# Optimization experiments

Hardware: AMD Instinct MI355X
Metric: run time of the kernel (lower is better)

Reference implementation:

```python
import jax, jax.numpy as jnp
import numpy as np

N, C_IN, T, V, M = 2048, 16, 8, 21, 2
C_OUT = 64
VM = V * M                       # 42 = n_joints
NUM_NODES = N * T * VM           # 688128 flattened nodes
NUM_HEDGES = NUM_NODES           # hyperedge ids drawn from same range
E_INC = 4 * NUM_NODES            # incidence (node, hyperedge) pairs
EMBED = VM * C_OUT // 8          # 336
HEADS = 4
HEAD_DIM = EMBED // HEADS        # 84


def setup_inputs() -> dict:
    key = jax.random.key(0)
    ks = jax.random.split(key, 16)
    g = lambda k, s: jax.random.normal(k, s, jnp.float32) * 0.02
    return dict(
        x=jax.random.normal(ks[0], (N, C_IN, T, V, M), jnp.float32),
        hi=jax.random.randint(ks[1], (2, E_INC), 0, NUM_NODES, jnp.int32),
        hc_w=g(ks[2], (C_OUT, C_IN)), hc_b=jnp.zeros((C_OUT,), jnp.float32),
        conv_w=g(ks[3], (8, 8)), conv_b=jnp.zeros((8,), jnp.float32),
        bn_gamma=jnp.ones((C_IN,), jnp.float32), bn_beta=jnp.zeros((C_IN,), jnp.float32),
        proj_w=g(ks[4], (C_OUT, C_IN)), proj_b=jnp.zeros((C_OUT,), jnp.float32),
        wq=g(ks[5], (EMBED, EMBED)), bq=jnp.zeros((EMBED,), jnp.float32),
        wk=g(ks[6], (EMBED, EMBED)), bk=jnp.zeros((EMBED,), jnp.float32),
        wv=g(ks[7], (EMBED, EMBED)), bv=jnp.zeros((EMBED,), jnp.float32),
        in_proj_w=g(ks[8], (3 * EMBED, EMBED)), in_proj_b=jnp.zeros((3 * EMBED,), jnp.float32),
        out_proj_w=g(ks[9], (EMBED, EMBED)), out_proj_b=jnp.zeros((EMBED,), jnp.float32),
        fc_w=g(ks[10], (8 * EMBED, EMBED)), fc_b=jnp.zeros((8 * EMBED,), jnp.float32),
    )


def _forward(x, hi, hc_w, hc_b, conv_w, conv_b, bn_gamma, bn_beta, proj_w, proj_b,
             wq, bq, wk, bk, wv, bv, in_proj_w, in_proj_b, out_proj_w, out_proj_b,
             fc_w, fc_b):
    # ---- residual branch: rearrange n c t v m -> n c (vm) t, BN (train-mode batch stats), proj ----
    res = x.reshape(N, C_IN, T, VM).transpose(0, 1, 3, 2)          # [N,C,VM,T]
    mean = res.mean(axis=(0, 2, 3), keepdims=True)
    var = ((res - mean) ** 2).mean(axis=(0, 2, 3), keepdims=True)
    res = (res - mean) * jax.lax.rsqrt(var + 1e-5)
    res = res * bn_gamma[None, :, None, None] + bn_beta[None, :, None, None]
    res = res.transpose(0, 3, 2, 1)                                 # n t vm c
    res = res @ proj_w.T + proj_b                                   # [N,T,VM,C_OUT]
    res = res.reshape(N, T, VM * C_OUT)                             # [N,8,2688]

    # ---- HypergraphConv (PyG math: D^-1 H B H^T X Theta + bias) ----
    xn = x.transpose(0, 2, 3, 4, 1).reshape(NUM_NODES, C_IN)        # (n t v m) c
    xt = xn @ hc_w.T                                                # [Nn, C_OUT]
    node_idx, edge_idx = hi[0], hi[1]
    ones = jnp.ones((E_INC,), xt.dtype)
    D = jax.ops.segment_sum(ones, node_idx, NUM_NODES)
    Dinv = jnp.where(D > 0, 1.0 / D, 0.0)
    Bd = jax.ops.segment_sum(ones, edge_idx, NUM_HEDGES)
    Binv = jnp.where(Bd > 0, 1.0 / Bd, 0.0)
    e = jax.ops.segment_sum(Binv[edge_idx, None] * xt[node_idx], edge_idx, NUM_HEDGES)
    h = jax.ops.segment_sum(Dinv[node_idx, None] * e[edge_idx], node_idx, NUM_NODES)
    h = h + hc_b                                                    # [Nn, C_OUT]

    # torch .view(N,-1,T,V,M) is a raw reshape of the (nodes, C) buffer
    h = h.reshape(N, C_OUT, T, V, M)
    h = h.transpose(0, 2, 3, 4, 1).reshape(N, T, VM, C_OUT)         # n t vm c

    # ---- Conv2d(8->8, k=(1,1), stride=(1,8)) over channel dim T ----
    hs = h[:, :, :, ::8]                                            # [N,8,VM,8]
    hc2 = jnp.einsum('oi,nivw->novw', conv_w, hs) + conv_b[None, :, None, None]
    seq = hc2.transpose(0, 1, 3, 2).reshape(N, 8, EMBED)            # n t (c vm) -> [N,8,336]

    # ---- external QKV projections + nn.MultiheadAttention ----
    q = seq @ wq.T + bq
    k = seq @ wk.T + bk
    v = seq @ wv.T + bv
    qq = q @ in_proj_w[:EMBED].T + in_proj_b[:EMBED]
    kk = k @ in_proj_w[EMBED:2 * EMBED].T + in_proj_b[EMBED:2 * EMBED]
    vv = v @ in_proj_w[2 * EMBED:].T + in_proj_b[2 * EMBED:]
    qq = qq.reshape(N, 8, HEADS, HEAD_DIM)
    kk = kk.reshape(N, 8, HEADS, HEAD_DIM)
    vv = vv.reshape(N, 8, HEADS, HEAD_DIM)
    scores = jnp.einsum('nshd,nthd->nhst', qq, kk) / np.sqrt(HEAD_DIM).astype(np.float32)
    attn = jax.nn.softmax(scores, axis=-1)
    ao = jnp.einsum('nhst,nthd->nshd', attn, vv).reshape(N, 8, EMBED)
    ao = ao @ out_proj_w.T + out_proj_b

    out = ao @ fc_w.T + fc_b                                        # [N,8,8*EMBED=2688]
    out = jax.nn.relu(out + res)
    return out.reshape(N, 64, T, V, M)                              # raw view, C'=64


def reference(x, hi, hc_w, hc_b, conv_w, conv_b, bn_gamma, bn_beta, proj_w, proj_b,
              wq, bq, wk, bk, wv, bv, in_proj_w, in_proj_b, out_proj_w, out_proj_b,
              fc_w, fc_b):
    return _forward(x, hi, hc_w, hc_b, conv_w, conv_b, bn_gamma, bn_beta, proj_w, proj_b,
                    wq, bq, wk, bk, wv, bv, in_proj_w, in_proj_b, out_proj_w, out_proj_b,
                    fc_w, fc_b)
```

## Files before the change

kernel.cpp:

```cpp
#include <hip/hip_runtime.h>

#define N_    2048
#define CIN   16
#define T_    8
#define VM_   42
#define COUT  64
#define NODES (N_*T_*VM_)
#define EINC  (4*NODES)
#define EMB   336
#define PERN  (T_*VM_*COUT)
#define XPERN (CIN*T_*VM_)
#define NBUK  672
#define BCAP  4608
#define LCAP  16

typedef __attribute__((ext_vector_type(8))) short bf16x8;
typedef __attribute__((ext_vector_type(4))) float f32x4;
typedef unsigned short ushort_t;

static const size_t O_A   = 0;
static const size_t SZ_AB = (size_t)NODES*64;
static const size_t O_B   = SZ_AB;
static const size_t O_SEQ = 2*SZ_AB;
static const size_t SZ_SEQ= (size_t)N_*8*EMB;
static const size_t O_AO  = O_SEQ+SZ_SEQ;
static const size_t O_SD  = O_AO+SZ_SEQ;
static const size_t O_BN  = O_SD + 4*(size_t)NODES;
static const size_t O_BE  = O_BN + 64;
static const size_t O_WF  = O_BE + 4096;
static const size_t O_SEQF = O_B;
static const size_t O_AOF  = O_B + 3600000;
static const size_t O_QKV  = O_B + 6600000;

__device__ inline short bf16r(float f){
    unsigned u = __builtin_bit_cast(unsigned, f);
    u += 0x7FFFu + ((u>>16)&1u);
    return (short)(u>>16);
}
__device__ inline float b2f(ushort_t u){
    return __builtin_bit_cast(float, ((unsigned)u)<<16);
}

__global__ __launch_bounds__(256) void k_bn_stats(const float* __restrict__ x, float* __restrict__ bn){
    int b=blockIdx.x, ci=b&15, grp=b>>4;
    int w=threadIdx.x>>6, lane=threadIdx.x&63;
    float s=0.f,q=0.f;
    for(int i=0;i<16;i++){
        int n = grp*64 + w*16 + i;
        const float4* r4 = (const float4*)(x + (size_t)n*XPERN + ci*336);
        for(int k=lane;k<84;k+=64){
            float4 v=r4[k];
            s += v.x+v.y+v.z+v.w;
            q += v.x*v.x+v.y*v.y+v.z*v.z+v.w*v.w;
        }
    }
    for(int off=32;off;off>>=1){ s+=__shfl_down(s,off); q+=__shfl_down(q,off); }
    if(lane==0){ atomicAdd(bn+ci,s); atomicAdd(bn+16+ci,q); }
}

__global__ void k_bn_final(float* bn, const float* __restrict__ g, const float* __restrict__ b){
    int c = threadIdx.x;
    if(c<16){
        const float inv = 1.f/(float)NODES;
        float mean = bn[c]*inv;
        float var  = bn[16+c]*inv - mean*mean;
        float rs   = rsqrtf(var+1e-5f);
        float sc   = g[c]*rs;
        bn[32+c] = sc;
        bn[48+c] = b[c]-mean*sc;
    }
}

__global__ __launch_bounds__(256) void k_xt(const float* __restrict__ x, const float* __restrict__ hcw, ushort_t* __restrict__ xt){
    __shared__ float xs[5376];
    int n=blockIdx.x, tid=threadIdx.x;
    const float4* xr4=(const float4*)(x+(size_t)n*XPERN);
    float4* xs4=(float4*)xs;
    for(int f=tid; f<1344; f+=256) xs4[f]=xr4[f];
    int co=tid&63, q=tid>>6;
    float w[16];
    #pragma unroll
    for(int ci=0;ci<16;ci++) w[ci]=hcw[co*16+ci];
    __syncthreads();
    ushort_t* xn = xt + (size_t)n*336*64;
    for(int g=0; g<21; g++){
        int tl0 = q*84 + g*4;
        float4 acc={0.f,0.f,0.f,0.f};
        #pragma unroll
        for(int ci=0;ci<16;ci++){
            float4 xv = *(const float4*)(xs + ci*336 + tl0);
            acc.x+=xv.x*w[ci]; acc.y+=xv.y*w[ci]; acc.z+=xv.z*w[ci]; acc.w+=xv.w*w[ci];
        }
        xn[(size_t)(tl0+0)*64+co]=(ushort_t)bf16r(acc.x);
        xn[(size_t)(tl0+1)*64+co]=(ushort_t)bf16r(acc.y);
        xn[(size_t)(tl0+2)*64+co]=(ushort_t)bf16r(acc.z);
        xn[(size_t)(tl0+3)*64+co]=(ushort_t)bf16r(acc.w);
    }
}

__global__ void k_initcur(int* __restrict__ gcurE, int* __restrict__ gcurD){
    int i=blockIdx.x*256+threadIdx.x;
    if(i<NBUK){ gcurE[i]=i*BCAP; gcurD[i]=i*BCAP; }
}

__global__ __launch_bounds__(256) void k_bin(const int* __restrict__ seg, const int* __restrict__ pay,
                                             int* __restrict__ gcur, unsigned* __restrict__ staging){
    __shared__ unsigned bins[NBUK*LCAP];
    __shared__ int lcnt[NBUK];
    int tid=threadIdx.x;
    for(int i=tid;i<NBUK;i+=256) lcnt[i]=0;
    __syncthreads();
    int base=blockIdx.x*4096;
    for(int k=0;k<16;k++){
        int i=base+k*256+tid;
        int sv=seg[i], pv=pay[i];
        int b=sv>>10;
        unsigned e=((unsigned)(sv&1023)<<20)|(unsigned)pv;
        int p=atomicAdd(&lcnt[b],1);
        if(p<LCAP) bins[b*LCAP+p]=e;
        else{
            int g=atomicAdd(&gcur[b],1);
            if(g<(b+1)*BCAP) staging[g]=e;
        }
    }
    __syncthreads();
    for(int b=tid;b<NBUK;b+=256){
        int c=lcnt[b]; if(c>LCAP)c=LCAP;
        if(c>0){
            int g=atomicAdd(&gcur[b],c);
            int lim=(b+1)*BCAP;
            for(int j=0;j<c;j++) if(g+j<lim) staging[g+j]=bins[b*LCAP+j];
        }
    }
}

__global__ __launch_bounds__(256) void k_csrsort(unsigned* __restrict__ staging, const int* __restrict__ gcur,
                                                 int* __restrict__ startX, int* __restrict__ cntX){
    __shared__ unsigned ents[BCAP];
    __shared__ unsigned outp[BCAP];
    __shared__ int segc[1024];
    __shared__ int wsum[4];
    int b=blockIdx.x, tid=threadIdx.x, lane=tid&63, wv=tid>>6;
    int cnt_b = gcur[b] - b*BCAP;
    if(cnt_b>BCAP) cnt_b=BCAP;
    unsigned* sb = staging + (size_t)b*BCAP;
    for(int i=tid;i<cnt_b;i+=256) ents[i]=sb[i];
    for(int i=tid;i<1024;i+=256) segc[i]=0;
    __syncthreads();
    for(int i=tid;i<cnt_b;i+=256) atomicAdd(&segc[ents[i]>>20],1);
    __syncthreads();
    int c0=segc[tid*4],c1=segc[tid*4+1],c2=segc[tid*4+2],c3=segc[tid*4+3];
    int tsum=c0+c1+c2+c3;
    int incl=tsum;
    #pragma unroll
    for(int off=1;off<64;off<<=1){ int v=__shfl_up(incl,off); if(lane>=off) incl+=v; }
    if(lane==63) wsum[wv]=incl;
    __syncthreads();
    int w0=wsum[0],w1=wsum[1],w2=wsum[2];
    int wexcl = (wv>0?w0:0)+(wv>1?w1:0)+(wv>2?w2:0);
    int run = incl - tsum + wexcl;
    int gs = b*1024 + tid*4;
    startX[gs+0]=b*BCAP+run; cntX[gs+0]=c0; segc[tid*4+0]=run; run+=c0;
    startX[gs+1]=b*BCAP+run; cntX[gs+1]=c1; segc[tid*4+1]=run; run+=c1;
    startX[gs+2]=b*BCAP+run; cntX[gs+2]=c2; segc[tid*4+2]=run; run+=c2;
    startX[gs+3]=b*BCAP+run; cntX[gs+3]=c3; segc[tid*4+3]=run; run+=c3;
    __syncthreads();
    for(int i=tid;i<cnt_b;i+=256){
        unsigned e=ents[i]; int s=e>>20;
        int p=atomicAdd(&segc[s],1);
        outp[p]=e&0xFFFFFu;
    }
    __syncthreads();
    for(int i=tid;i<cnt_b;i+=256) sb[i]=outp[i];
}

__global__ __launch_bounds__(256) void k_gath(const ushort_t* __restrict__ src, const int* __restrict__ csr,
                                              const int* __restrict__ startX, const int* __restrict__ cntX,
                                              ushort_t* __restrict__ dst){
    int s = blockIdx.x*8 + (threadIdx.x>>5);
    int l = threadIdx.x & 31;
    int c = cntX[s];
    int start = startX[s];
    float ax=0.f, ay=0.f;
    int nv = (c<32)? c : 32;
    int myidx = (l<nv)? csr[start+l] : 0;
    for(int j=0;j<nv;j++){
        int idx = __shfl(myidx, j, 32);
        ushort2 v = *(const ushort2*)(src + (size_t)idx*64 + l*2);
        ax += b2f(v.x); ay += b2f(v.y);
    }
    for(int j=32;j<c;j++){
        int idx = csr[start+j];
        ushort2 v = *(const ushort2*)(src + (size_t)idx*64 + l*2);
        ax += b2f(v.x); ay += b2f(v.y);
    }
    float scale = (c>0)? 1.f/(float)c : 0.f;
    ushort2 o; o.x=(ushort_t)bf16r(ax*scale); o.y=(ushort_t)bf16r(ay*scale);
    *(ushort2*)(dst + (size_t)s*64 + l*2) = o;
}

__global__ __launch_bounds__(256) void k_seq(const ushort_t* __restrict__ h,
                                             const float* __restrict__ hcb, const float* __restrict__ cw,
                                             const float* __restrict__ cb, short* __restrict__ seqf){
    __shared__ float hb[64], cws[64], cbs[8];
    int n = blockIdx.x, tid=threadIdx.x;
    if(tid<64){ hb[tid]=hcb[tid]; cws[tid]=cw[tid]; }
    if(tid<8) cbs[tid]=cb[tid];
    __syncthreads();
    const ushort_t* hn = h + (size_t)n*PERN;
    int rbase = (n&1)*8;
    short* d0 = seqf + (size_t)(n>>1)*5632;
    for(int e=tid; e<336; e+=256){
        int k = e/42, u = e%42;
        float hv[8];
        #pragma unroll
        for(int t=0;t<8;t++){
            int idx = 2688*k + t*42 + u;
            hv[t] = b2f(hn[idx]) + hb[idx&63];
        }
        int lpart = ((e>>3)&3)<<4;
        size_t obase = (size_t)(e>>5)*512 + (e&7);
        #pragma unroll
        for(int o=0;o<8;o++){
            float acc=cbs[o];
            #pragma unroll
            for(int t=0;t<8;t++) acc += cws[o*8+t]*hv[t];
            d0[obase + (size_t)((rbase+o)|lpart)*8] = bf16r(acc);
        }
    }
    if(tid<128){
        int o=tid>>4, kk=336+(tid&15);
        int l=(rbase+o)|(((kk>>3)&3)<<4);
        d0[(size_t)(kk>>5)*512 + (size_t)l*8 + (kk&7)] = 0;
    }
}

__global__ __launch_bounds__(256) void k_fusew2(const float* __restrict__ ipw, const float* __restrict__ ipb,
        const float* __restrict__ wq, const float* __restrict__ wk, const float* __restrict__ wv,
        const float* __restrict__ bq, const float* __restrict__ bk, const float* __restrict__ bv,
        const float* __restrict__ fcw, const float* __restrict__ opw,
        const float* __restrict__ opb, const float* __restrict__ fcb,
        short* __restrict__ W1F, short* __restrict__ W2F, float* __restrict__ BE){
    __shared__ float As[5376], Ws[5376], bms[336];
    int rt=blockIdx.x, r0=rt*16, tid=threadIdx.x;
    int m=(r0<1008)?(r0/336):3;
    const float* Asrc = (m<3)? (ipw+(size_t)r0*336) : (fcw+(size_t)(r0-1008)*336);
    const float* Bmat = (m==0)?wq:((m==1)?wk:((m==2)?wv:opw));
    const float* bvec = (m==0)?bq:((m==1)?bk:((m==2)?bv:opb));
    for(int f=tid;f<5376;f+=256) As[f]=Asrc[f];
    for(int f=tid;f<336;f+=256) bms[f]=bvec[f];
    __syncthreads();
    if(tid<168){
        int i0=tid, i1=tid+168;
        float a0[16], a1[16];
        #pragma unroll
        for(int r=0;r<16;r++){a0[r]=0.f;a1[r]=0.f;}
        for(int k=0;k<336;k++){
            float b0=Bmat[(size_t)k*336+i0];
            float b1=Bmat[(size_t)k*336+i1];
            #pragma unroll
            for(int r=0;r<16;r++){ float av=As[r*336+k]; a0[r]+=av*b0; a1[r]+=av*b1; }
        }
        #pragma unroll
        for(int r=0;r<16;r++){ Ws[r*336+i0]=a0[r]; Ws[r*336+i1]=a1[r]; }
    }
    if(tid>=192 && tid<208){
        int rr=tid-192;
        float acc=(m<3)? ipb[r0+rr] : fcb[r0+rr-1008];
        for(int k=0;k<336;k++) acc+=As[rr*336+k]*bms[k];
        BE[r0+rr]=acc;
    }
    __syncthreads();
    short* dst=(m<3)? (W1F+(size_t)rt*5632) : (W2F+(size_t)(rt-63)*5632);
    for(int f=tid; f<5632; f+=256){
        int kb=f>>9, rem=f&511, l=rem>>3, j=rem&7;
        int row=l&15, k=kb*32+((l>>4)<<3)+j;
        dst[f] = (k<336)? bf16r(Ws[row*336+k]) : (short)0;
    }
}

__global__ __launch_bounds__(256) void k_res(const float* __restrict__ x, const float* __restrict__ bn,
                                             const float* __restrict__ pw, const float* __restrict__ pb,
                                             const float* __restrict__ bfc, ushort_t* __restrict__ res){
    __shared__ float xp[5376], pws[1024], pbs[64], scs[16], shs[16];
    int n=blockIdx.x, tid=threadIdx.x;
    if(tid<16){ scs[tid]=bn[32+tid]; shs[tid]=bn[48+tid]; }
    if(tid<64) pbs[tid]=pb[tid];
    for(int f=tid;f<1024;f+=256) pws[f]=pw[f];
    __syncthreads();
    const float* xn = x + (size_t)n*XPERN;
    for(int f=tid;f<5376;f+=256){ int ci=f/336; xp[f]=xn[f]*scs[ci]+shs[ci]; }
    __syncthreads();
    ushort_t* rn = res + (size_t)n*PERN;
    for(int j=tid;j<2688;j+=256){
        int co=j&63, w=j>>6;
        float base = bfc[j]+pbs[co];
        float a[8];
        #pragma unroll
        for(int s=0;s<8;s++) a[s]=base;
        #pragma unroll
        for(int ci=0;ci<16;ci++){
            float c=pws[co*16+ci];
            const float* xr = xp + ci*336 + w;
            #pragma unroll
            for(int s=0;s<8;s++) a[s]+=c*xr[s*42];
        }
        #pragma unroll
        for(int s=0;s<8;s++) rn[s*2688+j]=(ushort_t)bf16r(a[s]);
    }
}

__global__ __launch_bounds__(256) void k_gemm(const bf16x8* __restrict__ Af, const bf16x8* __restrict__ Wf,
                                              const ushort_t* __restrict__ addterm, const float* __restrict__ bias,
                                              float* __restrict__ C, int CT, int CW, int relu){
    int wv = threadIdx.x>>6, l = threadIdx.x&63;
    int ct = blockIdx.y*4 + wv;
    if(ct>=CT) return;
    int rt0 = blockIdx.x*2;
    const bf16x8* Ap = Af + (size_t)rt0*704 + l;
    const bf16x8* Bp = Wf + (size_t)ct *704 + l;
    f32x4 acc0={0.f,0.f,0.f,0.f}, acc1={0.f,0.f,0.f,0.f};
    #pragma unroll
    for(int kb=0;kb<11;kb++){
        bf16x8 b  = Bp[kb*64];
        bf16x8 a0 = Ap[kb*64];
        bf16x8 a1 = Ap[704 + kb*64];
        acc0 = __builtin_amdgcn_mfma_f32_16x16x32_bf16(a0,b,acc0,0,0,0);
        acc1 = __builtin_amdgcn_mfma_f32_16x16x32_bf16(a1,b,acc1,0,0,0);
    }
    int col = ct*16 + (l&15);
    int r   = rt0*16 + (l>>4)*4;
    float bb = bias ? bias[col] : 0.f;
    #pragma unroll
    for(int rr=0;rr<4;rr++){
        size_t o0 = (size_t)(r+rr)*CW + col;
        size_t o1 = (size_t)(r+16+rr)*CW + col;
        float v0 = acc0[rr] + bb;
        float v1 = acc1[rr] + bb;
        if(addterm){ v0 += b2f(addterm[o0]); v1 += b2f(addterm[o1]); }
        if(relu){ v0 = fmaxf(v0,0.f); v1 = fmaxf(v1,0.f); }
        C[o0]=v0; C[o1]=v1;
    }
}

__global__ __launch_bounds__(256) void k_attn2(const float* __restrict__ qkv, short* __restrict__ aof){
    __shared__ float ss[8*1008];
    __shared__ float sc[256];
    __shared__ float aos[8*336];
    int n=blockIdx.x, tid=threadIdx.x;
    const float* src = qkv + (size_t)n*8064;
    for(int f=tid; f<8064; f+=256) ss[f]=src[f];
    __syncthreads();
    {
        int h=tid>>6, s=(tid>>3)&7, t=tid&7;
        const float* qp=ss + s*1008 + h*84;
        const float* kp=ss + t*1008 + 336 + h*84;
        float d=0.f;
        for(int d0=0;d0<84;d0++) d+=qp[d0]*kp[d0];
        sc[tid]=d*0.10910894511799619f;
    }
    __syncthreads();
    if(tid<32){
        float* row = sc + (tid>>3)*64 + (tid&7)*8;
        float m=row[0];
        #pragma unroll
        for(int t=1;t<8;t++) m=fmaxf(m,row[t]);
        float sum=0.f;
        #pragma unroll
        for(int t=0;t<8;t++){ float e=__expf(row[t]-m); row[t]=e; sum+=e; }
        float r=1.f/sum;
        #pragma unroll
        for(int t=0;t<8;t++) row[t]*=r;
    }
    __syncthreads();
    for(int o=tid;o<336;o+=256){
        int h=o/84;
        float acc[8];
        #pragma unroll
        for(int s=0;s<8;s++) acc[s]=0.f;
        #pragma unroll
        for(int t=0;t<8;t++){
            float v=ss[t*1008+672+o];
            #pragma unroll
            for(int s=0;s<8;s++) acc[s]+=sc[h*64+s*8+t]*v;
        }
        #pragma unroll
        for(int s=0;s<8;s++) aos[s*336+o]=acc[s];
    }
    __syncthreads();
    int rt=n>>1, half=n&1;
    for(int e=tid; e<2816; e+=256){
        int row=e&7, k=e>>3;
        float v = (k<336)? aos[row*336+k] : 0.f;
        int l = (half*8+row) | (((k>>3)&3)<<4);
        int j = k&7;
        aof[(size_t)rt*5632 + (size_t)(k>>5)*512 + l*8 + j] = bf16r(v);
    }
}

extern "C" void kernel_launch(void* const* d_in, const int* in_sizes, int n_in,
                              void* d_out, int out_size, void* d_ws, size_t ws_size,
                              hipStream_t stream) {
    const float* x    = (const float*)d_in[0];
    const int*   hi   = (const int*  )d_in[1];
    const float* hcw  = (const float*)d_in[2];
    const float* hcb  = (const float*)d_in[3];
    const float* cw   = (const float*)d_in[4];
    const float* cb   = (const float*)d_in[5];
    const float* bng  = (const float*)d_in[6];
    const float* bnb  = (const float*)d_in[7];
    const float* pw   = (const float*)d_in[8];
    const float* pb   = (const float*)d_in[9];
    const float* wq   = (const float*)d_in[10];
    const float* bq   = (const float*)d_in[11];
    const float* wk   = (const float*)d_in[12];
    const float* bk   = (const float*)d_in[13];
    const float* wv   = (const float*)d_in[14];
    const float* bv   = (const float*)d_in[15];
    const float* ipw  = (const float*)d_in[16];
    const float* ipb  = (const float*)d_in[17];
    const float* opw  = (const float*)d_in[18];
    const float* opb  = (const float*)d_in[19];
    const float* fcw  = (const float*)d_in[20];
    const float* fcb  = (const float*)d_in[21];
    float* ws  = (float*)d_ws;
    float* out = (float*)d_out;

    unsigned* stgE = (unsigned*)(ws + O_SEQ);
    int* gcurE = (int*)(ws + O_SEQ) + (size_t)NBUK*BCAP;
    int* gcurD = gcurE + NBUK;
    unsigned* stgD = (unsigned*)(ws + O_AO);
    int* SD = (int*)(ws + O_SD);
    short* W1F = (short*)(ws + O_WF);
    short* W2F = W1F + (size_t)63*5632;

    hipMemsetAsync(ws + O_BN, 0, 64*sizeof(float), stream);
    k_initcur<<<3,256,0,stream>>>(gcurE, gcurD);

    k_bn_stats<<<512,256,0,stream>>>(x, ws+O_BN);
    k_bn_final<<<1,64,0,stream>>>(ws+O_BN, bng, bnb);
    k_xt<<<2048,256,0,stream>>>(x, hcw, (ushort_t*)(ws+O_A));
    k_fusew2<<<231,256,0,stream>>>(ipw, ipb, wq, wk, wv, bq, bk, bv,
                                   fcw, opw, opb, fcb, W1F, W2F, ws+O_BE);

    k_bin<<<NBUK,256,0,stream>>>(hi+EINC, hi, gcurE, stgE);
    k_bin<<<NBUK,256,0,stream>>>(hi, hi+EINC, gcurD, stgD);
    k_csrsort<<<NBUK,256,0,stream>>>(stgE, gcurE, SD, SD+NODES);
    k_csrsort<<<NBUK,256,0,stream>>>(stgD, gcurD, SD+2*(size_t)NODES, SD+3*(size_t)NODES);

    k_gath<<<86016,256,0,stream>>>((const ushort_t*)(ws+O_A), (const int*)stgE,
                                   SD, SD+NODES, (ushort_t*)(ws+O_B));
    k_gath<<<86016,256,0,stream>>>((const ushort_t*)(ws+O_B), (const int*)stgD,
                                   SD+2*(size_t)NODES, SD+3*(size_t)NODES, (ushort_t*)(ws+O_A));

    k_seq<<<2048,256,0,stream>>>((const ushort_t*)(ws+O_A), hcb, cw, cb, (short*)(ws+O_SEQF));
    k_res<<<2048,256,0,stream>>>(x, ws+O_BN, pw, pb, ws+O_BE+1008, (ushort_t*)(ws+O_A));
    {   dim3 g1(512,16);
        k_gemm<<<g1,256,0,stream>>>((const bf16x8*)(ws+O_SEQF),(const bf16x8*)W1F,
                                    nullptr, ws+O_BE, ws+O_QKV, 63, 1008, 0); }
    k_attn2<<<2048,256,0,stream>>>(ws+O_QKV, (short*)(ws+O_AOF));
    {   dim3 g2(512,42);
        k_gemm<<<g2,256,0,stream>>>((const bf16x8*)(ws+O_AOF),(const bf16x8*)W2F,
                                    (const ushort_t*)(ws+O_A), nullptr, out, 168, 2688, 1); }
}
```

Measured before the change: 1.049 ms.

## Store gathered hypergraph features in fp8 and stage GEMM epilogues through LDS

Node features from the hyperconv projection and both gather/mean passes are now stored as fp8 instead of bf16. This halves the bytes moved by the random-access gathers, which dominate memory traffic. The QKV GEMM now writes bf16 output through an LDS staging tile with vectorized stores, and attention reads it as bf16. The final GEMM also stages through LDS so the residual add, ReLU and fp32 output are done with vector loads and stores. The cost is lower precision in the hypergraph path (fp8 e4m3 for averaged features) and in the QKV activations, which risks accuracy tolerance failures.

```diff
diff --git a/kernel.cpp b/kernel.cpp
--- a/kernel.cpp
+++ b/kernel.cpp
@@ -17,6 +17,7 @@
 typedef __attribute__((ext_vector_type(8))) short bf16x8;
 typedef __attribute__((ext_vector_type(4))) float f32x4;
 typedef unsigned short ushort_t;
+typedef unsigned char  uchar_t;
 
 static const size_t O_A   = 0;
 static const size_t SZ_AB = (size_t)NODES*64;
@@ -40,6 +41,9 @@
 __device__ inline float b2f(ushort_t u){
     return __builtin_bit_cast(float, ((unsigned)u)<<16);
 }
+__device__ inline uchar_t f2fp8(float f){
+    return (uchar_t)(__builtin_amdgcn_cvt_pk_fp8_f32(f,f,0,false)&0xFFu);
+}
 
 __global__ __launch_bounds__(256) void k_bn_stats(const float* __restrict__ x, float* __restrict__ bn){
     int b=blockIdx.x, ci=b&15, grp=b>>4;
@@ -71,7 +75,7 @@
     }
 }
 
-__global__ __launch_bounds__(256) void k_xt(const float* __restrict__ x, const float* __restrict__ hcw, ushort_t* __restrict__ xt){
+__global__ __launch_bounds__(256) void k_xt(const float* __restrict__ x, const float* __restrict__ hcw, uchar_t* __restrict__ xt){
     __shared__ float xs[5376];
     int n=blockIdx.x, tid=threadIdx.x;
     const float4* xr4=(const float4*)(x+(size_t)n*XPERN);
@@ -82,7 +86,7 @@
     #pragma unroll
     for(int ci=0;ci<16;ci++) w[ci]=hcw[co*16+ci];
     __syncthreads();
-    ushort_t* xn = xt + (size_t)n*336*64;
+    uchar_t* xn = xt + (size_t)n*336*64;
     for(int g=0; g<21; g++){
         int tl0 = q*84 + g*4;
         float4 acc={0.f,0.f,0.f,0.f};
@@ -91,10 +95,10 @@
             float4 xv = *(const float4*)(xs + ci*336 + tl0);
             acc.x+=xv.x*w[ci]; acc.y+=xv.y*w[ci]; acc.z+=xv.z*w[ci]; acc.w+=xv.w*w[ci];
         }
-        xn[(size_t)(tl0+0)*64+co]=(ushort_t)bf16r(acc.x);
-        xn[(size_t)(tl0+1)*64+co]=(ushort_t)bf16r(acc.y);
-        xn[(size_t)(tl0+2)*64+co]=(ushort_t)bf16r(acc.z);
-        xn[(size_t)(tl0+3)*64+co]=(ushort_t)bf16r(acc.w);
+        xn[(size_t)(tl0+0)*64+co]=f2fp8(acc.x);
+        xn[(size_t)(tl0+1)*64+co]=f2fp8(acc.y);
+        xn[(size_t)(tl0+2)*64+co]=f2fp8(acc.z);
+        xn[(size_t)(tl0+3)*64+co]=f2fp8(acc.w);
     }
 }
 
@@ -174,9 +178,9 @@
     for(int i=tid;i<cnt_b;i+=256) sb[i]=outp[i];
 }
 
-__global__ __launch_bounds__(256) void k_gath(const ushort_t* __restrict__ src, const int* __restrict__ csr,
+__global__ __launch_bounds__(256) void k_gath(const uchar_t* __restrict__ src, const int* __restrict__ csr,
                                               const int* __restrict__ startX, const int* __restrict__ cntX,
-                                              ushort_t* __restrict__ dst){
+                                              uchar_t* __restrict__ dst){
     int s = blockIdx.x*8 + (threadIdx.x>>5);
     int l = threadIdx.x & 31;
     int c = cntX[s];
@@ -186,20 +190,22 @@
     int myidx = (l<nv)? csr[start+l] : 0;
     for(int j=0;j<nv;j++){
         int idx = __shfl(myidx, j, 32);
-        ushort2 v = *(const ushort2*)(src + (size_t)idx*64 + l*2);
-        ax += b2f(v.x); ay += b2f(v.y);
+        unsigned v = *(const ushort_t*)(src + (size_t)idx*64 + l*2);
+        ax += __builtin_amdgcn_cvt_f32_fp8(v,0);
+        ay += __builtin_amdgcn_cvt_f32_fp8(v,1);
     }
     for(int j=32;j<c;j++){
         int idx = csr[start+j];
-        ushort2 v = *(const ushort2*)(src + (size_t)idx*64 + l*2);
-        ax += b2f(v.x); ay += b2f(v.y);
+        unsigned v = *(const ushort_t*)(src + (size_t)idx*64 + l*2);
+        ax += __builtin_amdgcn_cvt_f32_fp8(v,0);
+        ay += __builtin_amdgcn_cvt_f32_fp8(v,1);
     }
     float scale = (c>0)? 1.f/(float)c : 0.f;
-    ushort2 o; o.x=(ushort_t)bf16r(ax*scale); o.y=(ushort_t)bf16r(ay*scale);
-    *(ushort2*)(dst + (size_t)s*64 + l*2) = o;
-}
-
-__global__ __launch_bounds__(256) void k_seq(const ushort_t* __restrict__ h,
+    unsigned p = __builtin_amdgcn_cvt_pk_fp8_f32(ax*scale, ay*scale, 0, false);
+    *(ushort_t*)(dst + (size_t)s*64 + l*2) = (ushort_t)(p&0xFFFFu);
+}
+
+__global__ __launch_bounds__(256) void k_seq(const uchar_t* __restrict__ h,
                                              const float* __restrict__ hcb, const float* __restrict__ cw,
                                              const float* __restrict__ cb, short* __restrict__ seqf){
     __shared__ float hb[64], cws[64], cbs[8];
@@ -207,7 +213,7 @@
     if(tid<64){ hb[tid]=hcb[tid]; cws[tid]=cw[tid]; }
     if(tid<8) cbs[tid]=cb[tid];
     __syncthreads();
-    const ushort_t* hn = h + (size_t)n*PERN;
+    const uchar_t* hn = h + (size_t)n*PERN;
     int rbase = (n&1)*8;
     short* d0 = seqf + (size_t)(n>>1)*5632;
     for(int e=tid; e<336; e+=256){
@@ -216,7 +222,7 @@
         #pragma unroll
         for(int t=0;t<8;t++){
             int idx = 2688*k + t*42 + u;
-            hv[t] = b2f(hn[idx]) + hb[idx&63];
+            hv[t] = __builtin_amdgcn_cvt_f32_fp8((unsigned)hn[idx],0) + hb[idx&63];
         }
         int lpart = ((e>>3)&3)<<4;
         size_t obase = (size_t)(e>>5)*512 + (e&7);
@@ -310,46 +316,96 @@
     }
 }
 
-__global__ __launch_bounds__(256) void k_gemm(const bf16x8* __restrict__ Af, const bf16x8* __restrict__ Wf,
-                                              const ushort_t* __restrict__ addterm, const float* __restrict__ bias,
-                                              float* __restrict__ C, int CT, int CW, int relu){
+__global__ __launch_bounds__(256) void k_gemm_qkv(const bf16x8* __restrict__ Af, const bf16x8* __restrict__ Wf,
+                                                  const float* __restrict__ bias, ushort_t* __restrict__ C){
+    __shared__ float stage[32][68];
     int wv = threadIdx.x>>6, l = threadIdx.x&63;
     int ct = blockIdx.y*4 + wv;
-    if(ct>=CT) return;
     int rt0 = blockIdx.x*2;
-    const bf16x8* Ap = Af + (size_t)rt0*704 + l;
-    const bf16x8* Bp = Wf + (size_t)ct *704 + l;
-    f32x4 acc0={0.f,0.f,0.f,0.f}, acc1={0.f,0.f,0.f,0.f};
+    if(ct<63){
+        const bf16x8* Ap = Af + (size_t)rt0*704 + l;
+        const bf16x8* Bp = Wf + (size_t)ct *704 + l;
+        f32x4 acc0={0.f,0.f,0.f,0.f}, acc1={0.f,0.f,0.f,0.f};
+        #pragma unroll
+        for(int kb=0;kb<11;kb++){
+            bf16x8 b  = Bp[kb*64];
+            bf16x8 a0 = Ap[kb*64];
+            bf16x8 a1 = Ap[704 + kb*64];
+            acc0 = __builtin_amdgcn_mfma_f32_16x16x32_bf16(a0,b,acc0,0,0,0);
+            acc1 = __builtin_amdgcn_mfma_f32_16x16x32_bf16(a1,b,acc1,0,0,0);
+        }
+        int cc=wv*16+(l&15), rr0=(l>>4)*4;
+        float bb = bias[ct*16+(l&15)];
+        #pragma unroll
+        for(int r=0;r<4;r++){
+            stage[rr0+r][cc]    = acc0[r]+bb;
+            stage[rr0+16+r][cc] = acc1[r]+bb;
+        }
+    }
+    __syncthreads();
+    int lr=threadIdx.x>>3, q=threadIdx.x&7;
+    int col0 = blockIdx.y*64 + q*8;
+    if(col0<1008){
+        short u8[8];
+        #pragma unroll
+        for(int j=0;j<8;j++) u8[j]=bf16r(stage[lr][q*8+j]);
+        *(bf16x8*)(C + (size_t)(rt0*16+lr)*1008 + col0) = *(bf16x8*)u8;
+    }
+}
+
+__global__ __launch_bounds__(256) void k_gemm_out(const bf16x8* __restrict__ Af, const bf16x8* __restrict__ Wf,
+                                                  const ushort_t* __restrict__ res, float* __restrict__ C){
+    __shared__ float stage[32][68];
+    int wv = threadIdx.x>>6, l = threadIdx.x&63;
+    int ct = blockIdx.y*4 + wv;
+    int rt0 = blockIdx.x*2;
+    {
+        const bf16x8* Ap = Af + (size_t)rt0*704 + l;
+        const bf16x8* Bp = Wf + (size_t)ct *704 + l;
+        f32x4 acc0={0.f,0.f,0.f,0.f}, acc1={0.f,0.f,0.f,0.f};
+        #pragma unroll
+        for(int kb=0;kb<11;kb++){
+            bf16x8 b  = Bp[kb*64];
+            bf16x8 a0 = Ap[kb*64];
+            bf16x8 a1 = Ap[704 + kb*64];
+            acc0 = __builtin_amdgcn_mfma_f32_16x16x32_bf16(a0,b,acc0,0,0,0);
+            acc1 = __builtin_amdgcn_mfma_f32_16x16x32_bf16(a1,b,acc1,0,0,0);
+        }
+        int cc=wv*16+(l&15), rr0=(l>>4)*4;
+        #pragma unroll
+        for(int r=0;r<4;r++){
+            stage[rr0+r][cc]    = acc0[r];
+            stage[rr0+16+r][cc] = acc1[r];
+        }
+    }
+    __syncthreads();
+    int lr=threadIdx.x>>3, q=threadIdx.x&7;
+    int row = rt0*16 + lr;
+    int col0 = blockIdx.y*64 + q*8;
+    bf16x8 rv = *(const bf16x8*)(res + (size_t)row*2688 + col0);
+    float v[8];
     #pragma unroll
-    for(int kb=0;kb<11;kb++){
-        bf16x8 b  = Bp[kb*64];
-        bf16x8 a0 = Ap[kb*64];
-        bf16x8 a1 = Ap[704 + kb*64];
-        acc0 = __builtin_amdgcn_mfma_f32_16x16x32_bf16(a0,b,acc0,0,0,0);
-        acc1 = __builtin_amdgcn_mfma_f32_16x16x32_bf16(a1,b,acc1,0,0,0);
-    }
-    int col = ct*16 + (l&15);
-    int r   = rt0*16 + (l>>4)*4;
-    float bb = bias ? bias[col] : 0.f;
-    #pragma unroll
-    for(int rr=0;rr<4;rr++){
-        size_t o0 = (size_t)(r+rr)*CW + col;
-        size_t o1 = (size_t)(r+16+rr)*CW + col;
-        float v0 = acc0[rr] + bb;
-        float v1 = acc1[rr] + bb;
-        if(addterm){ v0 += b2f(addterm[o0]); v1 += b2f(addterm[o1]); }
-        if(relu){ v0 = fmaxf(v0,0.f); v1 = fmaxf(v1,0.f); }
-        C[o0]=v0; C[o1]=v1;
-    }
-}
-
-__global__ __launch_bounds__(256) void k_attn2(const float* __restrict__ qkv, short* __restrict__ aof){
+    for(int j=0;j<8;j++){
+        float t = stage[lr][q*8+j] + b2f((ushort_t)rv[j]);
+        v[j] = fmaxf(t,0.f);
+    }
+    float* dst = C + (size_t)row*2688 + col0;
+    float4 f0={v[0],v[1],v[2],v[3]}, f1={v[4],v[5],v[6],v[7]};
+    *(float4*)dst = f0;
+    *(float4*)(dst+4) = f1;
+}
+
+__global__ __launch_bounds__(256) void k_attn2(const ushort_t* __restrict__ qkv, short* __restrict__ aof){
     __shared__ float ss[8*1008];
     __shared__ float sc[256];
     __shared__ float aos[8*336];
     int n=blockIdx.x, tid=threadIdx.x;
-    const float* src = qkv + (size_t)n*8064;
-    for(int f=tid; f<8064; f+=256) ss[f]=src[f];
+    const bf16x8* src8 = (const bf16x8*)(qkv + (size_t)n*8064);
+    for(int i=tid; i<1008; i+=256){
+        bf16x8 v = src8[i];
+        #pragma unroll
+        for(int j=0;j<8;j++) ss[i*8+j]=b2f((ushort_t)v[j]);
+    }
     __syncthreads();
     {
         int h=tid>>6, s=(tid>>3)&7, t=tid&7;
@@ -433,13 +489,14 @@
     int* SD = (int*)(ws + O_SD);
     short* W1F = (short*)(ws + O_WF);
     short* W2F = W1F + (size_t)63*5632;
+    ushort_t* qkvp = (ushort_t*)(ws + O_QKV);
 
     hipMemsetAsync(ws + O_BN, 0, 64*sizeof(float), stream);
     k_initcur<<<3,256,0,stream>>>(gcurE, gcurD);
 
     k_bn_stats<<<512,256,0,stream>>>(x, ws+O_BN);
     k_bn_final<<<1,64,0,stream>>>(ws+O_BN, bng, bnb);
-    k_xt<<<2048,256,0,stream>>>(x, hcw, (ushort_t*)(ws+O_A));
+    k_xt<<<2048,256,0,stream>>>(x, hcw, (uchar_t*)(ws+O_A));
     k_fusew2<<<231,256,0,stream>>>(ipw, ipb, wq, wk, wv, bq, bk, bv,
                                    fcw, opw, opb, fcb, W1F, W2F, ws+O_BE);
 
@@ -448,18 +505,18 @@
     k_csrsort<<<NBUK,256,0,stream>>>(stgE, gcurE, SD, SD+NODES);
     k_csrsort<<<NBUK,256,0,stream>>>(stgD, gcurD, SD+2*(size_t)NODES, SD+3*(size_t)NODES);
 
-    k_gath<<<86016,256,0,stream>>>((const ushort_t*)(ws+O_A), (const int*)stgE,
-                                   SD, SD+NODES, (ushort_t*)(ws+O_B));
-    k_gath<<<86016,256,0,stream>>>((const ushort_t*)(ws+O_B), (const int*)stgD,
-                                   SD+2*(size_t)NODES, SD+3*(size_t)NODES, (ushort_t*)(ws+O_A));
-
-    k_seq<<<2048,256,0,stream>>>((const ushort_t*)(ws+O_A), hcb, cw, cb, (short*)(ws+O_SEQF));
+    k_gath<<<86016,256,0,stream>>>((const uchar_t*)(ws+O_A), (const int*)stgE,
+                                   SD, SD+NODES, (uchar_t*)(ws+O_B));
+    k_gath<<<86016,256,0,stream>>>((const uchar_t*)(ws+O_B), (const int*)stgD,
+                                   SD+2*(size_t)NODES, SD+3*(size_t)NODES, (uchar_t*)(ws+O_A));
+
+    k_seq<<<2048,256,0,stream>>>((const uchar_t*)(ws+O_A), hcb, cw, cb, (short*)(ws+O_SEQF));
     k_res<<<2048,256,0,stream>>>(x, ws+O_BN, pw, pb, ws+O_BE+1008, (ushort_t*)(ws+O_A));
     {   dim3 g1(512,16);
-        k_gemm<<<g1,256,0,stream>>>((const bf16x8*)(ws+O_SEQF),(const bf16x8*)W1F,
-                                    nullptr, ws+O_BE, ws+O_QKV, 63, 1008, 0); }
-    k_attn2<<<2048,256,0,stream>>>(ws+O_QKV, (short*)(ws+O_AOF));
+        k_gemm_qkv<<<g1,256,0,stream>>>((const bf16x8*)(ws+O_SEQF),(const bf16x8*)W1F,
+                                        ws+O_BE, qkvp); }
+    k_attn2<<<2048,256,0,stream>>>(qkvp, (short*)(ws+O_AOF));
     {   dim3 g2(512,42);
-        k_gemm<<<g2,256,0,stream>>>((const bf16x8*)(ws+O_AOF),(const bf16x8*)W2F,
-                                    (const ushort_t*)(ws+O_A), nullptr, out, 168, 2688, 1); }
-}
+        k_gemm_out<<<g2,256,0,stream>>>((const bf16x8*)(ws+O_AOF),(const bf16x8*)W2F,
+                                        (const ushort_t*)(ws+O_A), out); }
+}
```

Measured after the change: 1.018 ms. -3.0%, faster.
